# Kernel tuning notes

Measured on AMD Instinct MI355X. Metric: run time of the kernel, lower is better.

Reference implementation:

```python
import jax, jax.numpy as jnp
import numpy as np

B, S, DM, H = 8, 1024, 256, 8
D = DM // H  # 32


def setup_inputs() -> dict:
    key = jax.random.key(0)
    ks = jax.random.split(key, 8)
    xav = (6.0 / (DM + DM)) ** 0.5  # xavier_uniform bound for square Linear
    return {
        "q": jax.random.normal(ks[0], (B, S, DM), jnp.float32),
        "k": jax.random.normal(ks[1], (B, S, DM), jnp.float32),
        "v": jax.random.normal(ks[2], (B, S, DM), jnp.float32),
        "mask": jnp.tril(jnp.ones((1, 1, S, S), jnp.int32)),  # causal: mask==0 is disallowed
        "zero_pad": 1,
        "k_index": 5,
        "Wk": jax.random.uniform(ks[3], (DM, DM), jnp.float32, -xav, xav),
        "bk": jnp.zeros((DM,), jnp.float32),
        "Wv": jax.random.uniform(ks[4], (DM, DM), jnp.float32, -xav, xav),
        "bv": jnp.zeros((DM,), jnp.float32),
        "Wo": jax.random.uniform(ks[5], (DM, DM), jnp.float32, -xav, xav),
        "bo": jnp.zeros((DM,), jnp.float32),
    }


def _attention4sparse_kt(qh, kh, vh, mask, zero_pad, k_index):
    # qh/kh/vh: [B,H,S,D]; mask: [1,1,S,S]
    d = qh.shape[-1]
    scores = jnp.einsum("bhid,bhjd->bhij", qh, kh) / jnp.sqrt(jnp.float32(d))
    scores = jnp.where(mask == 0, jnp.float32(-1e32), scores)
    attn = jax.nn.softmax(scores, axis=-1)  # [B,H,S,S]
    seqlen = attn.shape[2]
    if k_index + 1 < seqlen:
        # per-row k_index-th largest prob as threshold; keep top-k_index entries, re-softmax
        thresh = jax.lax.top_k(attn, k_index)[0][..., -1:]  # [B,H,S,1]
        sparse = jnp.where(attn - thresh >= 0.0, attn, jnp.float32(-1e16))
        resoft = jax.nn.softmax(sparse, axis=-1)
        rows = jnp.arange(seqlen)[None, None, :, None]
        # rows 0..k_index keep the original softmax; later rows use sparsified re-softmax
        attn = jnp.where(rows <= k_index, attn, resoft)
    if zero_pad:
        attn = attn.at[:, :, 0, :].set(0.0)
    out = jnp.einsum("bhij,bhjd->bhid", attn, vh)
    return out, attn


def reference(q, k, v, mask, zero_pad, k_index, Wk, bk, Wv, bv, Wo, bo):
    bs = q.shape[0]
    # key_query_same=True: q and k share k_linear
    kh = (k @ Wk.T + bk).reshape(bs, -1, H, D).transpose(0, 2, 1, 3)
    qh = (q @ Wk.T + bk).reshape(bs, -1, H, D).transpose(0, 2, 1, 3)
    vh = (v @ Wv.T + bv).reshape(bs, -1, H, D).transpose(0, 2, 1, 3)
    out, attn = _attention4sparse_kt(qh, kh, vh, mask, zero_pad, k_index)
    concat = out.transpose(0, 2, 1, 3).reshape(bs, -1, DM)
    output = concat @ Wo.T + bo
    return output, attn
```

## Files before the change

### kernel.cpp

```cpp
#include <hip/hip_runtime.h>
#include <cfloat>
#include <cmath>

#define S_LEN  1024
#define DHEAD  32
#define NHEAD  8
#define DMODEL 256

template<int MODE>
__global__ __launch_bounds__(256)
void gemm128x64(const float* __restrict__ X0, const float* __restrict__ X1,
                const float* __restrict__ X2,
                const float* __restrict__ WA, const float* __restrict__ bA,
                const float* __restrict__ WB, const float* __restrict__ bB,
                float* __restrict__ C0, float* __restrict__ C1, float* __restrict__ C2)
{
    __shared__ float Xs[128*36];
    __shared__ float Ws_[64*36];
    const float* X; const float* W; const float* bias; float* C;
    if (MODE == 0) {
        const int z = blockIdx.z;
        X    = (z==0) ? X0 : ((z==1) ? X1 : X2);
        W    = (z==2) ? WB : WA;
        bias = (z==2) ? bB : bA;
        C    = (z==0) ? C0 : ((z==1) ? C1 : C2);
    } else { X = X0; W = WA; bias = bA; C = C0; }

    const int tid  = threadIdx.x;
    const int row0 = blockIdx.x * 128;
    const int col0 = blockIdx.y * 64;
    const int tx = tid & 15, ty = tid >> 4;
    const int sr = tid >> 1, shf = tid & 1;
    const int wc = tid >> 2, wq = tid & 3;

    float acc[8][4];
    #pragma unroll
    for (int a = 0; a < 8; ++a)
        #pragma unroll
        for (int b = 0; b < 4; ++b) acc[a][b] = 0.f;

    const int xg   = ty & 7;
    const int wg2  = (tx >> 1) & 7;
    const int swbx = (sr >> 3) & 7;
    const int swbw = (wc >> 3) & 7;

    for (int k0 = 0; k0 < DMODEL; k0 += 32) {
        const float4* xp = (const float4*)(X + (size_t)(row0 + sr) * DMODEL + k0 + shf*16);
        const float4* wp = (const float4*)(W + (size_t)(col0 + wc) * DMODEL + k0 + wq*8);
        float4 xv[4], wv[2];
        #pragma unroll
        for (int q4 = 0; q4 < 4; ++q4) xv[q4] = xp[q4];
        #pragma unroll
        for (int q2 = 0; q2 < 2; ++q2) wv[q2] = wp[q2];
        if (k0) __syncthreads();
        #pragma unroll
        for (int q4 = 0; q4 < 4; ++q4) {
            const int slot = (shf*4 + q4) ^ swbx;
            *(float4*)&Xs[sr*36 + slot*4] = xv[q4];
        }
        #pragma unroll
        for (int q2 = 0; q2 < 2; ++q2) {
            const int slot = (wq*2 + q2) ^ swbw;
            *(float4*)&Ws_[wc*36 + slot*4] = wv[q2];
        }
        __syncthreads();
        #pragma unroll
        for (int g = 0; g < 8; ++g) {
            float4 xf[8];
            #pragma unroll
            for (int ri = 0; ri < 8; ++ri)
                xf[ri] = *(const float4*)&Xs[(ty*8+ri)*36 + ((g ^ xg) << 2)];
            #pragma unroll
            for (int ci = 0; ci < 4; ++ci) {
                const float4 wf = *(const float4*)&Ws_[(tx*4+ci)*36 + ((g ^ wg2) << 2)];
                #pragma unroll
                for (int ri = 0; ri < 8; ++ri) {
                    acc[ri][ci] += xf[ri].x * wf.x;
                    acc[ri][ci] += xf[ri].y * wf.y;
                    acc[ri][ci] += xf[ri].z * wf.z;
                    acc[ri][ci] += xf[ri].w * wf.w;
                }
            }
        }
    }

    const int c = col0 + tx*4;
    const float4 bv4 = *(const float4*)(bias + c);
    #pragma unroll
    for (int ri = 0; ri < 8; ++ri) {
        const int r = row0 + ty*8 + ri;
        float4 o;
        o.x = acc[ri][0] + bv4.x; o.y = acc[ri][1] + bv4.y;
        o.z = acc[ri][2] + bv4.z; o.w = acc[ri][3] + bv4.w;
        if (MODE == 0) {
            const int bI = r >> 10, s = r & 1023;
            const int h = c >> 5, d0 = c & 31;
            *(float4*)(C + (((size_t)(bI*NHEAD + h))*S_LEN + s)*DHEAD + d0) = o;
        } else {
            *(float4*)(C + (size_t)r * DMODEL + c) = o;
        }
    }
}

__device__ __forceinline__ float process_row_v3(
    float (&e_)[4][4], const int i, const int l, const int kidx, const int zp,
    const float* __restrict__ vbase, float* __restrict__ arow)
{
    const int vcol = l & 31;
    float m = -FLT_MAX;
    #pragma unroll
    for (int t = 0; t < 4; ++t)
        #pragma unroll
        for (int e = 0; e < 4; ++e) m = fmaxf(m, e_[t][e]);
    #pragma unroll
    for (int off = 32; off >= 1; off >>= 1) m = fmaxf(m, __shfl_xor(m, off, 64));

    float Z = 0.f;
    #pragma unroll
    for (int t = 0; t < 4; ++t)
        #pragma unroll
        for (int e = 0; e < 4; ++e) { const float x = expf(e_[t][e] - m); e_[t][e] = x; Z += x; }
    #pragma unroll
    for (int off = 32; off >= 1; off >>= 1) Z += __shfl_xor(Z, off, 64);

    float tk[8];
    #pragma unroll
    for (int u = 0; u < 8; ++u) tk[u] = -FLT_MAX;
    #pragma unroll
    for (int t = 0; t < 4; ++t)
        #pragma unroll
        for (int e = 0; e < 4; ++e) {
            const float v = e_[t][e];
            if (v > tk[7]) {
                float w = v;
                #pragma unroll
                for (int u = 0; u < 8; ++u) {
                    const float mx = fmaxf(tk[u], w);
                    const float mn = fminf(tk[u], w);
                    tk[u] = mx; w = mn;
                }
            }
        }
    float te = -FLT_MAX;
    for (int round = 0; round < kidx; ++round) {
        float g = tk[0];
        #pragma unroll
        for (int off = 32; off >= 1; off >>= 1) g = fmaxf(g, __shfl_xor(g, off, 64));
        te = g;
        const unsigned long long bb = __ballot(tk[0] == g);
        const int leader = (int)__ffsll(bb) - 1;
        if (l == leader) {
            tk[0]=tk[1]; tk[1]=tk[2]; tk[2]=tk[3]; tk[3]=tk[4];
            tk[4]=tk[5]; tk[5]=tk[6]; tk[6]=tk[7]; tk[7]=-FLT_MAX;
        }
    }

    const float rZ = 1.0f / Z;
    const bool  sparse = (i > kidx);
    const bool  zr = (i == 0) && (zp != 0);
    float wgt[4][4];
    if (sparse) {
        const float pth = te / Z;
        const float tlo = te - te * 2.4e-7f;
        float S2 = 0.f;
        #pragma unroll
        for (int t = 0; t < 4; ++t)
            #pragma unroll
            for (int e = 0; e < 4; ++e) {
                const float ev = e_[t][e];
                bool sel = (ev >= te);
                if (!sel && ev >= tlo) {
                    sel = ((ev / Z) >= pth);
                }
                const float x = expf(ev * rZ - rZ);
                const float xs = sel ? x : 0.f;
                e_[t][e] = xs;
                S2 += xs;
            }
        #pragma unroll
        for (int off = 32; off >= 1; off >>= 1) S2 += __shfl_xor(S2, off, 64);
        const float rS2 = 1.0f / S2;
        #pragma unroll
        for (int t = 0; t < 4; ++t)
            #pragma unroll
            for (int e = 0; e < 4; ++e) wgt[t][e] = e_[t][e] * rS2;
    } else {
        #pragma unroll
        for (int t = 0; t < 4; ++t)
            #pragma unroll
            for (int e = 0; e < 4; ++e) wgt[t][e] = zr ? 0.f : e_[t][e] * rZ;
    }

    #pragma unroll
    for (int t = 0; t < 4; ++t) {
        float4 f; f.x = wgt[t][0]; f.y = wgt[t][1]; f.z = wgt[t][2]; f.w = wgt[t][3];
        *(float4*)(arow + t*256 + 4*l) = f;
    }
    float o = 0.f;
    #pragma unroll
    for (int t = 0; t < 4; ++t)
        #pragma unroll
        for (int e = 0; e < 4; ++e) {
            unsigned long long mask = __ballot(wgt[t][e] != 0.f);
            while (mask) {
                const int src = (int)__ffsll(mask) - 1;
                mask &= mask - 1;
                const float wb = __shfl(wgt[t][e], src, 64);
                const int j = t*256 + 4*src + e;
                o += wb * vbase[(size_t)j * DHEAD + vcol];
            }
        }
    return o;
}

__global__ __launch_bounds__(512)
void attn_sparse_v3(const float* __restrict__ qh, const float* __restrict__ kh,
                    const float* __restrict__ vh,
                    const int* __restrict__ zp_p, const int* __restrict__ ki_p,
                    float* __restrict__ attn, float* __restrict__ outp)
{
    __shared__ float kT[2][32*264];
    const int tid = threadIdx.x;
    const int l = tid & 63, w = tid >> 6;
    const int g0 = blockIdx.x;
    const int bh = ((g0 & 7) << 3) + ((g0 >> 3) & 7);
    const int qb = g0 >> 6;
    const int i0 = qb * 16;
    const int iA = i0 + 2*w, iB = iA + 1;
    const int zp = zp_p[0];
    int kidx = ki_p[0];
    if (kidx < 1) kidx = 1;
    if (kidx > 8) kidx = 8;
    const float INVSCALE = 1.0f / sqrtf((float)DHEAD);

    const float* kb = kh + (size_t)bh * S_LEN * DHEAD;
    const float* vb = vh + (size_t)bh * S_LEN * DHEAD;

    float qa[32], qbr[32];
    {
        const float4* qpA = (const float4*)(qh + ((size_t)bh*S_LEN + iA)*DHEAD);
        const float4* qpB = (const float4*)(qh + ((size_t)bh*S_LEN + iB)*DHEAD);
        #pragma unroll
        for (int t4 = 0; t4 < 8; ++t4) {
            const float4 a = qpA[t4], b = qpB[t4];
            qa [t4*4+0]=a.x; qa [t4*4+1]=a.y; qa [t4*4+2]=a.z; qa [t4*4+3]=a.w;
            qbr[t4*4+0]=b.x; qbr[t4*4+1]=b.y; qbr[t4*4+2]=b.z; qbr[t4*4+3]=b.w;
        }
    }

    float sA[4][4], sB[4][4];
    #pragma unroll
    for (int t = 0; t < 4; ++t)
        #pragma unroll
        for (int e = 0; e < 4; ++e) { sA[t][e] = -FLT_MAX; sB[t][e] = -FLT_MAX; }

    const int nchunk = ((i0 + 15) >> 8) + 1;

    auto stage = [&](float* buf, int t) {
        const int jj = tid >> 1, hf = tid & 1;
        const float4* kp = (const float4*)(kb + ((size_t)(t*256 + jj))*DHEAD + hf*16);
        const float4 k0 = kp[0], k1 = kp[1], k2 = kp[2], k3 = kp[3];
        float* cb = buf + jj;
        const int rb = hf*16;
        cb[(rb+ 0)*264]=k0.x; cb[(rb+ 1)*264]=k0.y; cb[(rb+ 2)*264]=k0.z; cb[(rb+ 3)*264]=k0.w;
        cb[(rb+ 4)*264]=k1.x; cb[(rb+ 5)*264]=k1.y; cb[(rb+ 6)*264]=k1.z; cb[(rb+ 7)*264]=k1.w;
        cb[(rb+ 8)*264]=k2.x; cb[(rb+ 9)*264]=k2.y; cb[(rb+10)*264]=k2.z; cb[(rb+11)*264]=k2.w;
        cb[(rb+12)*264]=k3.x; cb[(rb+13)*264]=k3.y; cb[(rb+14)*264]=k3.z; cb[(rb+15)*264]=k3.w;
    };

    stage(kT[0], 0);
    #pragma unroll
    for (int t = 0; t < 4; ++t) {
        if (t < nchunk) {
            __syncthreads();
            if (t + 1 < nchunk) stage(kT[(t+1)&1], t+1);
            const float* buf = kT[t & 1];
            float dA[4] = {0.f,0.f,0.f,0.f}, dB[4] = {0.f,0.f,0.f,0.f};
            #pragma unroll
            for (int kk = 0; kk < 32; ++kk) {
                const float4 kv = *(const float4*)&buf[kk*264 + 4*l];
                dA[0] += qa[kk]*kv.x; dA[1] += qa[kk]*kv.y;
                dA[2] += qa[kk]*kv.z; dA[3] += qa[kk]*kv.w;
                dB[0] += qbr[kk]*kv.x; dB[1] += qbr[kk]*kv.y;
                dB[2] += qbr[kk]*kv.z; dB[3] += qbr[kk]*kv.w;
            }
            #pragma unroll
            for (int e = 0; e < 4; ++e) {
                const int j = t*256 + 4*l + e;
                if (j <= iA) sA[t][e] = dA[e] * INVSCALE;
                if (j <= iB) sB[t][e] = dB[e] * INVSCALE;
            }
        }
    }

    float* arowA = attn + ((size_t)bh*S_LEN + iA)*S_LEN;
    float* arowB = attn + ((size_t)bh*S_LEN + iB)*S_LEN;
    const float oA = process_row_v3(sA, iA, l, kidx, zp, vb, arowA);
    const float oB = process_row_v3(sB, iB, l, kidx, zp, vb, arowB);

    const int srow = iA + (l >> 5);
    const float oval = (l < 32) ? oA : oB;
    outp[((size_t)(bh >> 3)*S_LEN + srow)*DMODEL + (bh & 7)*DHEAD + (l & 31)] = oval;
}

extern "C" void kernel_launch(void* const* d_in, const int* in_sizes, int n_in,
                              void* d_out, int out_size, void* d_ws, size_t ws_size,
                              hipStream_t stream)
{
    (void)in_sizes; (void)n_in; (void)out_size; (void)ws_size;

    const float* q  = (const float*)d_in[0];
    const float* k  = (const float*)d_in[1];
    const float* v  = (const float*)d_in[2];
    const int*   zp = (const int*)d_in[4];
    const int*   ki = (const int*)d_in[5];
    const float* Wk = (const float*)d_in[6];
    const float* bk = (const float*)d_in[7];
    const float* Wv = (const float*)d_in[8];
    const float* bv = (const float*)d_in[9];
    const float* Wo = (const float*)d_in[10];
    const float* bo = (const float*)d_in[11];

    float* out  = (float*)d_out;
    float* attn = (float*)d_out + 2097152;

    float* ws   = (float*)d_ws;
    float* qh   = ws;
    float* kh   = ws + 2097152;
    float* vhp  = ws + 2*2097152;
    float* outp = ws + 3*2097152;

    hipLaunchKernelGGL((gemm128x64<0>), dim3(64, 4, 3), dim3(256), 0, stream,
                       q, k, v, Wk, bk, Wv, bv, qh, kh, vhp);

    hipLaunchKernelGGL(attn_sparse_v3, dim3(4096), dim3(512), 0, stream,
                       qh, kh, vhp, zp, ki, attn, outp);

    hipLaunchKernelGGL((gemm128x64<1>), dim3(64, 4, 1), dim3(256), 0, stream,
                       outp, nullptr, nullptr, Wo, bo, nullptr, nullptr,
                       out, nullptr, nullptr);
}
```

Before: 676.1 us.

## Use packed FMA and prefetch in GEMM, skip causal-masked work in sparse attention

The GEMM now accumulates with v_pk_fma_f32 on paired partial sums and prefetches the next K tile from global memory into registers while computing the current one. The attention row processing skips column groups beyond the causal limit, computes the re-softmax exp only for selected entries, and compacts the nonzero weights and their indices into per-wave shared buffers. The V accumulation then runs as a loop over that compacted list instead of a ballot/shuffle loop. This adds shared memory and caps the list at 144 entries, which could drop weights if ties produce more nonzeros, and the split accumulators change summation order.

```diff
diff --git a/kernel.cpp b/kernel.cpp
--- a/kernel.cpp
+++ b/kernel.cpp
@@ -6,6 +6,13 @@
 #define DHEAD  32
 #define NHEAD  8
 #define DMODEL 256
+
+typedef float f32x2 __attribute__((ext_vector_type(2)));
+typedef float f32x4 __attribute__((ext_vector_type(4)));
+
+__device__ __forceinline__ void pkfma(f32x2& d, f32x2 a, f32x2 b) {
+    asm("v_pk_fma_f32 %0, %1, %2, %0" : "+v"(d) : "v"(a), "v"(b));
+}
 
 template<int MODE>
 __global__ __launch_bounds__(256)
@@ -33,55 +40,61 @@
     const int sr = tid >> 1, shf = tid & 1;
     const int wc = tid >> 2, wq = tid & 3;
 
-    float acc[8][4];
+    f32x2 acc[8][4];
     #pragma unroll
     for (int a = 0; a < 8; ++a)
         #pragma unroll
-        for (int b = 0; b < 4; ++b) acc[a][b] = 0.f;
+        for (int b = 0; b < 4; ++b) acc[a][b] = (f32x2){0.f, 0.f};
 
     const int xg   = ty & 7;
     const int wg2  = (tx >> 1) & 7;
     const int swbx = (sr >> 3) & 7;
     const int swbw = (wc >> 3) & 7;
 
-    for (int k0 = 0; k0 < DMODEL; k0 += 32) {
+    float4 xv[4]; float4 wv[2];
+    auto gload = [&](int k0) {
         const float4* xp = (const float4*)(X + (size_t)(row0 + sr) * DMODEL + k0 + shf*16);
+        #pragma unroll
+        for (int q4 = 0; q4 < 4; ++q4) xv[q4] = xp[q4];
         const float4* wp = (const float4*)(W + (size_t)(col0 + wc) * DMODEL + k0 + wq*8);
-        float4 xv[4], wv[2];
-        #pragma unroll
-        for (int q4 = 0; q4 < 4; ++q4) xv[q4] = xp[q4];
         #pragma unroll
         for (int q2 = 0; q2 < 2; ++q2) wv[q2] = wp[q2];
-        if (k0) __syncthreads();
-        #pragma unroll
-        for (int q4 = 0; q4 < 4; ++q4) {
-            const int slot = (shf*4 + q4) ^ swbx;
-            *(float4*)&Xs[sr*36 + slot*4] = xv[q4];
-        }
-        #pragma unroll
-        for (int q2 = 0; q2 < 2; ++q2) {
-            const int slot = (wq*2 + q2) ^ swbw;
-            *(float4*)&Ws_[wc*36 + slot*4] = wv[q2];
-        }
-        __syncthreads();
+    };
+    auto lwrite = [&]() {
+        #pragma unroll
+        for (int q4 = 0; q4 < 4; ++q4)
+            *(float4*)&Xs[sr*36 + ((shf*4 + q4) ^ swbx)*4] = xv[q4];
+        #pragma unroll
+        for (int q2 = 0; q2 < 2; ++q2)
+            *(float4*)&Ws_[wc*36 + ((wq*2 + q2) ^ swbw)*4] = wv[q2];
+    };
+
+    gload(0); lwrite(); __syncthreads();
+
+    for (int t = 0; t < 8; ++t) {
+        if (t < 7) gload((t+1) * 32);
         #pragma unroll
         for (int g = 0; g < 8; ++g) {
-            float4 xf[8];
-            #pragma unroll
-            for (int ri = 0; ri < 8; ++ri)
-                xf[ri] = *(const float4*)&Xs[(ty*8+ri)*36 + ((g ^ xg) << 2)];
+            f32x2 xlo[8], xhi[8];
+            #pragma unroll
+            for (int ri = 0; ri < 8; ++ri) {
+                const f32x4 xf = *(const f32x4*)&Xs[(ty*8+ri)*36 + ((g ^ xg) << 2)];
+                xlo[ri] = __builtin_shufflevector(xf, xf, 0, 1);
+                xhi[ri] = __builtin_shufflevector(xf, xf, 2, 3);
+            }
             #pragma unroll
             for (int ci = 0; ci < 4; ++ci) {
-                const float4 wf = *(const float4*)&Ws_[(tx*4+ci)*36 + ((g ^ wg2) << 2)];
+                const f32x4 wf = *(const f32x4*)&Ws_[(tx*4+ci)*36 + ((g ^ wg2) << 2)];
+                const f32x2 wlo = __builtin_shufflevector(wf, wf, 0, 1);
+                const f32x2 whi = __builtin_shufflevector(wf, wf, 2, 3);
                 #pragma unroll
                 for (int ri = 0; ri < 8; ++ri) {
-                    acc[ri][ci] += xf[ri].x * wf.x;
-                    acc[ri][ci] += xf[ri].y * wf.y;
-                    acc[ri][ci] += xf[ri].z * wf.z;
-                    acc[ri][ci] += xf[ri].w * wf.w;
+                    pkfma(acc[ri][ci], xlo[ri], wlo);
+                    pkfma(acc[ri][ci], xhi[ri], whi);
                 }
             }
         }
+        if (t < 7) { __syncthreads(); lwrite(); __syncthreads(); }
     }
 
     const int c = col0 + tx*4;
@@ -90,8 +103,10 @@
     for (int ri = 0; ri < 8; ++ri) {
         const int r = row0 + ty*8 + ri;
         float4 o;
-        o.x = acc[ri][0] + bv4.x; o.y = acc[ri][1] + bv4.y;
-        o.z = acc[ri][2] + bv4.z; o.w = acc[ri][3] + bv4.w;
+        o.x = acc[ri][0].x + acc[ri][0].y + bv4.x;
+        o.y = acc[ri][1].x + acc[ri][1].y + bv4.y;
+        o.z = acc[ri][2].x + acc[ri][2].y + bv4.z;
+        o.w = acc[ri][3].x + acc[ri][3].y + bv4.w;
         if (MODE == 0) {
             const int bI = r >> 10, s = r & 1023;
             const int h = c >> 5, d0 = c & 31;
@@ -102,14 +117,17 @@
     }
 }
 
-__device__ __forceinline__ float process_row_v3(
+__device__ __forceinline__ float process_row_v4(
     float (&e_)[4][4], const int i, const int l, const int kidx, const int zp,
-    const float* __restrict__ vbase, float* __restrict__ arow)
+    const float* __restrict__ vbase, float* __restrict__ arow,
+    float* __restrict__ wbuf, unsigned short* __restrict__ jbuf)
 {
     const int vcol = l & 31;
+    const int ng = (i >> 8) + 1;
+
     float m = -FLT_MAX;
     #pragma unroll
-    for (int t = 0; t < 4; ++t)
+    for (int t = 0; t < 4; ++t) if (t < ng)
         #pragma unroll
         for (int e = 0; e < 4; ++e) m = fmaxf(m, e_[t][e]);
     #pragma unroll
@@ -117,9 +135,15 @@
 
     float Z = 0.f;
     #pragma unroll
-    for (int t = 0; t < 4; ++t)
-        #pragma unroll
-        for (int e = 0; e < 4; ++e) { const float x = expf(e_[t][e] - m); e_[t][e] = x; Z += x; }
+    for (int t = 0; t < 4; ++t) {
+        if (t < ng) {
+            #pragma unroll
+            for (int e = 0; e < 4; ++e) { const float x = expf(e_[t][e] - m); e_[t][e] = x; Z += x; }
+        } else {
+            #pragma unroll
+            for (int e = 0; e < 4; ++e) e_[t][e] = 0.f;
+        }
+    }
     #pragma unroll
     for (int off = 32; off >= 1; off >>= 1) Z += __shfl_xor(Z, off, 64);
 
@@ -127,7 +151,7 @@
     #pragma unroll
     for (int u = 0; u < 8; ++u) tk[u] = -FLT_MAX;
     #pragma unroll
-    for (int t = 0; t < 4; ++t)
+    for (int t = 0; t < 4; ++t) if (t < ng)
         #pragma unroll
         for (int e = 0; e < 4; ++e) {
             const float v = e_[t][e];
@@ -164,7 +188,7 @@
         const float tlo = te - te * 2.4e-7f;
         float S2 = 0.f;
         #pragma unroll
-        for (int t = 0; t < 4; ++t)
+        for (int t = 0; t < 4; ++t) if (t < ng)
             #pragma unroll
             for (int e = 0; e < 4; ++e) {
                 const float ev = e_[t][e];
@@ -172,8 +196,8 @@
                 if (!sel && ev >= tlo) {
                     sel = ((ev / Z) >= pth);
                 }
-                const float x = expf(ev * rZ - rZ);
-                const float xs = sel ? x : 0.f;
+                float xs = 0.f;
+                if (sel) xs = expf(ev * rZ - rZ);
                 e_[t][e] = xs;
                 S2 += xs;
             }
@@ -196,30 +220,44 @@
         float4 f; f.x = wgt[t][0]; f.y = wgt[t][1]; f.z = wgt[t][2]; f.w = wgt[t][3];
         *(float4*)(arow + t*256 + 4*l) = f;
     }
+
+    int n = 0;
+    #pragma unroll
+    for (int t = 0; t < 4; ++t) if (t < ng)
+        #pragma unroll
+        for (int e = 0; e < 4; ++e) {
+            const float pw = wgt[t][e];
+            const unsigned long long mk = __ballot(pw != 0.f);
+            if (pw != 0.f) {
+                const int pos = n + (int)__popcll(mk & ((1ull << l) - 1ull));
+                if (pos < 144) { jbuf[pos] = (unsigned short)(t*256 + 4*l + e); wbuf[pos] = pw; }
+            }
+            n += (int)__popcll(mk);
+        }
+    if (n > 144) n = 144;
+
     float o = 0.f;
-    #pragma unroll
-    for (int t = 0; t < 4; ++t)
-        #pragma unroll
-        for (int e = 0; e < 4; ++e) {
-            unsigned long long mask = __ballot(wgt[t][e] != 0.f);
-            while (mask) {
-                const int src = (int)__ffsll(mask) - 1;
-                mask &= mask - 1;
-                const float wb = __shfl(wgt[t][e], src, 64);
-                const int j = t*256 + 4*src + e;
-                o += wb * vbase[(size_t)j * DHEAD + vcol];
-            }
-        }
+    for (int q = 0; q < n; q += 4) {
+        #pragma unroll
+        for (int u = 0; u < 4; ++u) {
+            const int qq = q + u;
+            const int jj = (qq < n) ? (int)jbuf[qq] : 0;
+            const float ww = (qq < n) ? wbuf[qq] : 0.f;
+            o += ww * vbase[(size_t)jj * DHEAD + vcol];
+        }
+    }
     return o;
 }
 
 __global__ __launch_bounds__(512)
-void attn_sparse_v3(const float* __restrict__ qh, const float* __restrict__ kh,
+void attn_sparse_v4(const float* __restrict__ qh, const float* __restrict__ kh,
                     const float* __restrict__ vh,
                     const int* __restrict__ zp_p, const int* __restrict__ ki_p,
                     float* __restrict__ attn, float* __restrict__ outp)
 {
     __shared__ float kT[2][32*264];
+    __shared__ float wbuf[8*144];
+    __shared__ unsigned short jbuf[8*144];
     const int tid = threadIdx.x;
     const int l = tid & 63, w = tid >> 6;
     const int g0 = blockIdx.x;
@@ -295,8 +333,10 @@
 
     float* arowA = attn + ((size_t)bh*S_LEN + iA)*S_LEN;
     float* arowB = attn + ((size_t)bh*S_LEN + iB)*S_LEN;
-    const float oA = process_row_v3(sA, iA, l, kidx, zp, vb, arowA);
-    const float oB = process_row_v3(sB, iB, l, kidx, zp, vb, arowB);
+    float* wb = &wbuf[w*144];
+    unsigned short* jb = &jbuf[w*144];
+    const float oA = process_row_v4(sA, iA, l, kidx, zp, vb, arowA, wb, jb);
+    const float oB = process_row_v4(sB, iB, l, kidx, zp, vb, arowB, wb, jb);
 
     const int srow = iA + (l >> 5);
     const float oval = (l < 32) ? oA : oB;
@@ -333,7 +373,7 @@
     hipLaunchKernelGGL((gemm128x64<0>), dim3(64, 4, 3), dim3(256), 0, stream,
                        q, k, v, Wk, bk, Wv, bv, qh, kh, vhp);
 
-    hipLaunchKernelGGL(attn_sparse_v3, dim3(4096), dim3(512), 0, stream,
+    hipLaunchKernelGGL(attn_sparse_v4, dim3(4096), dim3(512), 0, stream,
                        qh, kh, vhp, zp, ki, attn, outp);
 
     hipLaunchKernelGGL((gemm128x64<1>), dim3(64, 4, 1), dim3(256), 0, stream,
```

Result: faster. 653.8 us (-3.3%).
